# Kernel tuning notes

Hardware: AMD Instinct MI355X
Metric: run time of the kernel (lower is better)

Reference implementation:

```python
import jax, jax.numpy as jnp
import numpy as np
from jax import lax

DIM = 32          # per-head dim of LiteMLA
HEADS = 8         # in_channels // dim = 256 // 32
C = 256           # in_channels = out_channels
EPS = 1e-15       # LiteMLA eps
BN_EPS = 1e-5


def hswish(x):
    return x * jnp.clip(x + 3.0, 0.0, 6.0) / 6.0


def bn(x, g, b, m, v):
    # eval-mode BatchNorm2d folded to per-channel scale/shift
    inv = g / jnp.sqrt(v + BN_EPS)
    return x * inv[None, :, None, None] + (b - m * inv)[None, :, None, None]


def dwconv(x, w):
    # depthwise conv, w: (C,1,k,k), stride 1, SAME padding (= padding k//2)
    return lax.conv_general_dilated(x, w, (1, 1), 'SAME',
                                    dimension_numbers=('NCHW', 'OIHW', 'NCHW'),
                                    feature_group_count=x.shape[1])


def relu_linear_att(qkv):
    # qkv: (B, h*3*DIM, H, W) with h = (1+num_scales)*HEADS
    B, Ctot, H, W = qkv.shape
    N = H * W
    qkv = qkv.reshape(B, -1, 3 * DIM, N)                 # (B,h,3d,N)
    q = jax.nn.relu(qkv[:, :, :DIM])                     # (B,h,d,N)
    k = jax.nn.relu(qkv[:, :, DIM:2 * DIM])
    v = qkv[:, :, 2 * DIM:]
    v = jnp.concatenate([v, jnp.ones_like(v[:, :, :1])], axis=2)  # (B,h,d+1,N)
    kv = jnp.einsum('bhdn,bhen->bhde', v, k)             # (B,h,d+1,d)
    out = jnp.einsum('bhde,bhen->bhdn', kv, q)           # (B,h,d+1,N)
    out = out[:, :, :-1] / (out[:, :, -1:] + EPS)        # normalize by denom row
    return out.reshape(B, -1, H, W)


def lite_mla(x, qkv_w, agg_dw_w, agg_pw_w, proj_w, proj_g, proj_b, proj_m, proj_v):
    qkv = jnp.einsum('bchw,oc->bohw', x, qkv_w)          # 1x1 conv -> (B,3C,H,W)
    d = dwconv(qkv, agg_dw_w)                            # depthwise 5x5
    B, _, H, W = d.shape
    g = 3 * HEADS                                        # 24 groups for grouped 1x1
    dg = d.reshape(B, g, -1, H, W)                       # (B,24,32,H,W)
    pw = jnp.einsum('bgihw,goi->bgohw', dg, agg_pw_w).reshape(B, -1, H, W)
    ms_qkv = jnp.concatenate([qkv, pw], axis=1)          # (B,6C,H,W)
    att = relu_linear_att(ms_qkv)                        # (B,2C,H,W)
    out = jnp.einsum('bchw,oc->bohw', att, proj_w)       # 1x1 proj, no bias
    return bn(out, proj_g, proj_b, proj_m, proj_v)


def mbconv(x, inv_w, inv_b, dwc_w, dwc_b, pw_w, pw_g, pw_b, pw_m, pw_v):
    h = hswish(jnp.einsum('bchw,oc->bohw', x, inv_w) + inv_b[None, :, None, None])
    h = hswish(dwconv(h, dwc_w) + dwc_b[None, :, None, None])
    h = jnp.einsum('bchw,oc->bohw', h, pw_w)
    return bn(h, pw_g, pw_b, pw_m, pw_v)


def setup_inputs() -> dict:
    key = jax.random.key(0)
    ks = jax.random.split(key, 12)
    B, H, W = 16, 32, 32
    mid = 4 * C
    return {
        "x": jax.random.normal(ks[0], (B, C, H, W), jnp.float32),
        "y": jax.random.normal(ks[1], (B, C, H, W), jnp.float32),
        "qkv_w": jax.random.normal(ks[2], (3 * C, C), jnp.float32) * 0.05,
        "agg_dw_w": jax.random.normal(ks[3], (3 * C, 1, 5, 5), jnp.float32) * 0.1,
        "agg_pw_w": jax.random.normal(ks[4], (3 * HEADS, C // HEADS, C // HEADS), jnp.float32) * 0.15,
        "proj_w": jax.random.normal(ks[5], (C, 2 * C), jnp.float32) * 0.04,
        "proj_g": jnp.ones((C,), jnp.float32),
        "proj_b": jnp.zeros((C,), jnp.float32),
        "proj_m": jax.random.normal(ks[6], (C,), jnp.float32) * 0.1,
        "proj_v": jnp.ones((C,), jnp.float32),
        "inv_w": jax.random.normal(ks[7], (mid, C), jnp.float32) * 0.06,
        "inv_b": jnp.zeros((mid,), jnp.float32),
        "dwc_w": jax.random.normal(ks[8], (mid, 1, 3, 3), jnp.float32) * 0.2,
        "dwc_b": jnp.zeros((mid,), jnp.float32),
        "pw_w": jax.random.normal(ks[9], (C, mid), jnp.float32) * 0.03,
        "pw_g": jnp.ones((C,), jnp.float32),
        "pw_b": jnp.zeros((C,), jnp.float32),
        "pw_m": jax.random.normal(ks[10], (C,), jnp.float32) * 0.1,
        "pw_v": jnp.ones((C,), jnp.float32),
    }


def reference(x, y, qkv_w, agg_dw_w, agg_pw_w, proj_w, proj_g, proj_b, proj_m, proj_v,
              inv_w, inv_b, dwc_w, dwc_b, pw_w, pw_g, pw_b, pw_m, pw_v):
    def block(t):
        # context module: residual LiteMLA
        t = t + lite_mla(t, qkv_w, agg_dw_w, agg_pw_w, proj_w, proj_g, proj_b, proj_m, proj_v)
        # local module: residual MBConv
        t = t + mbconv(t, inv_w, inv_b, dwc_w, dwc_b, pw_w, pw_g, pw_b, pw_m, pw_v)
        return t
    return block(x) + block(y)
```

## Files before the change

kernel.cpp:

```cpp
#include <hip/hip_runtime.h>
#include <cstddef>

#define NPIX 1024

static constexpr size_t WQKV_OFF  = 0;
static constexpr size_t WPROJ_OFF = 98304;
static constexpr size_t WINV_OFF  = 163840;
static constexpr size_t WPW_OFF   = 294912;
static constexpr size_t BXT_OFF   = 425984;
static constexpr size_t BQKV_OFF  = 4620288;
static constexpr size_t BDPW_OFF  = 17203200;
static constexpr size_t BATT_OFF  = 29786112;
static constexpr size_t BT1T_OFF  = 425984;
static constexpr size_t BH1T_OFF  = 4620288;
static constexpr size_t BH2T_OFF  = 21397504;
static constexpr size_t BATCH_NEED_F = 38174720;
static constexpr size_t XT_OFF    = 425984;
static constexpr size_t QKV_OFF   = 2523136;
static constexpr size_t DPW_OFF   = 8814592;
static constexpr size_t ATT_OFF   = 15106048;
static constexpr size_t T1_OFF    = 21463040;
static constexpr size_t T1T_OFF   = 25657344;
static constexpr size_t H1T_OFF   = 425984;
static constexpr size_t H2T_OFF   = 25657344;

typedef __attribute__((ext_vector_type(8))) short bf16x8;
typedef __attribute__((ext_vector_type(8))) unsigned short u16x8;
typedef __attribute__((ext_vector_type(4))) unsigned short u16x4;
typedef __attribute__((ext_vector_type(4))) float f32x4;

__device__ inline unsigned short f2bf(float f) {
    union { float f; unsigned int u; } v; v.f = f;
    unsigned int u = v.u;
    u += 0x7FFFu + ((u >> 16) & 1u);
    return (unsigned short)(u >> 16);
}
__device__ inline float bf2f(unsigned short u) {
    union { float f; unsigned int u; } v; v.u = ((unsigned int)u) << 16;
    return v.f;
}
__device__ inline u16x8 zero8() {
    u16x8 z = {0, 0, 0, 0, 0, 0, 0, 0};
    return z;
}

__global__ __launch_bounds__(256)
void wconv_all(const float* __restrict__ w0, const float* __restrict__ w1,
               const float* __restrict__ w2, const float* __restrict__ w3,
               unsigned short* __restrict__ d0, unsigned short* __restrict__ d1,
               unsigned short* __restrict__ d2, unsigned short* __restrict__ d3)
{
    const int bid = blockIdx.x;
    const float* W; unsigned short* WB; int O, K, base;
    if (bid < 96)       { W = w0; WB = d0; O = 768;  K = 256;  base = 0;   }
    else if (bid < 160) { W = w1; WB = d1; O = 256;  K = 512;  base = 96;  }
    else if (bid < 288) { W = w2; WB = d2; O = 1024; K = 256;  base = 160; }
    else                { W = w3; WB = d3; O = 256;  K = 1024; base = 288; }
    const int idx = (bid - base) * 256 + threadIdx.x;
    if (idx >= O * (K >> 3)) return;
    const int o = idx % O;
    const int koct = idx / O;
    u16x8 v;
#pragma unroll
    for (int j = 0; j < 8; j++) v[j] = f2bf(W[(size_t)o * K + koct * 8 + j]);
    *(u16x8*)(WB + ((size_t)koct * O + o) * 8) = v;
}

__global__ __launch_bounds__(256)
void xpose2(const float* __restrict__ X0, const float* __restrict__ X1,
            unsigned short* __restrict__ XT, const int C)
{
    __shared__ float tt[8][260];
    const int t = threadIdx.x;
    const int octs = C >> 3;
    const int strips = octs * 4;
    const int ib = blockIdx.x / strips;
    const int rem = blockIdx.x - ib * strips;
    const int coct = rem >> 2;
    const int n0 = (rem & 3) * 256;
    const float* src = (ib < 16) ? X0 + (size_t)ib * C * NPIX
                                 : X1 + (size_t)(ib - 16) * C * NPIX;
    const int cc = t >> 5;
    const int c8 = (t & 31) * 8;
    const float* xp = src + ((size_t)(coct * 8 + cc)) * NPIX + n0 + c8;
    *(float4*)(&tt[cc][c8])     = *(const float4*)(xp);
    *(float4*)(&tt[cc][c8 + 4]) = *(const float4*)(xp + 4);
    __syncthreads();
    u16x8 v;
#pragma unroll
    for (int j = 0; j < 8; j++) v[j] = f2bf(tt[j][t]);
    *(u16x8*)(XT + (((size_t)ib * octs + coct) * NPIX + n0 + t) * 8) = v;
}

template<int BM, int BN, int EPI, bool ACC, int OMODE>
__global__ __launch_bounds__(256)
void gemm_direct(const unsigned short* __restrict__ X, const unsigned short* __restrict__ X2,
                 const unsigned short* __restrict__ W,
                 float* __restrict__ Y, unsigned short* __restrict__ YB,
                 const int O, const int K,
                 const float* __restrict__ res, const float* __restrict__ res2,
                 const unsigned short* __restrict__ resb,
                 const float* __restrict__ bng, const float* __restrict__ bnb,
                 const float* __restrict__ bnm, const float* __restrict__ bnv,
                 const float* __restrict__ bias)
{
    constexpr int TN = NPIX / BN;
    constexpr int WAVES_N = (BN >= 128) ? 2 : 1;
    constexpr int WM = BM / (4 / WAVES_N);
    constexpr int MI = WM / 16;
    constexpr int NJ = 4;
    constexpr int DEPTH = (MI >= 4) ? 2 : ((EPI == 3 && MI >= 2) ? 2 : 4);

    const int t    = threadIdx.x;
    const int lane = t & 63;
    const int w    = t >> 6;

    const int gx  = gridDim.x;
    const int nwg = gx * gridDim.y;
    int bid = blockIdx.y * gx + blockIdx.x;
    bid = (bid & 7) * (nwg >> 3) + (bid >> 3);
    const int bx = bid % gx;
    const int by = bid / gx;

    const int o0 = bx * BM;
    const int b  = by / TN;
    const int n0 = (by % TN) * BN;

    const int wn = (WAVES_N == 2) ? (w & 1) * 64 : 0;
    const int wo = (WAVES_N == 2) ? (w >> 1) * WM : w * WM;

    const int l16 = lane & 15;
    const int lq  = lane >> 4;

    f32x4 acc[MI][NJ];
    f32x4 acc2[MI][NJ];
#pragma unroll
    for (int i = 0; i < MI; i++)
#pragma unroll
        for (int j = 0; j < NJ; j++) {
            f32x4 z = {0.f, 0.f, 0.f, 0.f};
            acc[i][j] = z;
            acc2[i][j] = z;
        }

    const unsigned short* Ab = W + ((size_t)lq * O + o0 + wo + l16) * 8;
    const size_t strideA = (size_t)O * 8;
    const size_t strideB = (size_t)NPIX * 8;
    const size_t boff = ((size_t)lq * NPIX + n0 + wn + l16) * 8;
    const int octs = K >> 3;

    auto ldA_ = [&](bf16x8* fr, int kb) {
#pragma unroll
        for (int i = 0; i < MI; i++)
            fr[i] = *(const bf16x8*)(Ab + (size_t)kb * strideA + i * 128);
    };
    auto ldB_ = [&](bf16x8* fr, const unsigned short* Bb, int kb) {
#pragma unroll
        for (int j = 0; j < NJ; j++)
            fr[j] = *(const bf16x8*)(Bb + (size_t)kb * strideB + j * 128);
    };
    auto domfma_ = [&](f32x4 (&ac)[MI][NJ], bf16x8* af, bf16x8* bf) {
#pragma unroll
        for (int i = 0; i < MI; i++)
#pragma unroll
            for (int j = 0; j < NJ; j++)
                ac[i][j] = __builtin_amdgcn_mfma_f32_16x16x32_bf16(
                    af[i], bf[j], ac[i][j], 0, 0, 0);
    };

    {
        const unsigned short* B1 = X + (size_t)b * K * NPIX + boff;
        const unsigned short* B2 = (EPI == 3)
            ? X2 + (size_t)b * K * NPIX + boff : nullptr;
        bf16x8 aS[DEPTH][MI], bS[DEPTH][NJ], qS[DEPTH][NJ];
#pragma unroll
        for (int d = 0; d < DEPTH; d++) {
            ldA_(aS[d], d * 4);
            ldB_(bS[d], B1, d * 4);
            if (EPI == 3) ldB_(qS[d], B2, d * 4);
        }
        for (int kb = 0; kb < octs; kb += 4 * DEPTH) {
#pragma unroll
            for (int d = 0; d < DEPTH; d++) {
                domfma_(acc, aS[d], bS[d]);
                if (EPI == 3) domfma_(acc2, aS[d], qS[d]);
                const int nxt = kb + (DEPTH + d) * 4;
                if (nxt < octs) {
                    ldA_(aS[d], nxt);
                    ldB_(bS[d], B1, nxt);
                    if (EPI == 3) ldB_(qS[d], B2, nxt);
                }
            }
        }
    }

    const int r0q = lq * 4;
    float scale[MI][4], shift[MI][4];
    if (EPI == 1 || EPI == 3) {
#pragma unroll
        for (int i = 0; i < MI; i++)
#pragma unroll
            for (int r = 0; r < 4; r++) {
                const int o = o0 + wo + i * 16 + r0q + r;
                const float inv = bng[o] / sqrtf(bnv[o] + 1e-5f);
                scale[i][r] = inv;
                shift[i][r] = bnb[o] - bnm[o] * inv;
            }
    } else if (EPI == 2) {
#pragma unroll
        for (int i = 0; i < MI; i++)
#pragma unroll
            for (int r = 0; r < 4; r++)
                shift[i][r] = bias[o0 + wo + i * 16 + r0q + r];
    }

#pragma unroll
    for (int i = 0; i < MI; i++) {
#pragma unroll
        for (int j = 0; j < NJ; j++) {
            const int nn = n0 + wn + j * 16 + l16;
            const int ob = wo + i * 16 + r0q;
            const size_t base = ((size_t)b * O + o0 + ob) * NPIX + nn;
            u16x4 r1v, r2v;
            if (EPI == 3) {
                const size_t ro = (((size_t)(b * 32 + ((o0 + ob) >> 3)) * NPIX + nn) * 8
                                   + ((o0 + ob) & 7));
                r1v = *(const u16x4*)(resb + ro);
                r2v = *(const u16x4*)(resb + (size_t)16 * 262144 + ro);
            }
            u16x4 p4;
#pragma unroll
            for (int r = 0; r < 4; r++) {
                const size_t off = base + (size_t)r * NPIX;
                float v = acc[i][j][r];
                if (EPI == 1) {
                    const float* rs = (b < 16) ? res : res2;
                    const size_t roff = ((size_t)(b & 15) * O + o0 + ob + r) * NPIX + nn;
                    v = v * scale[i][r] + shift[i][r] + rs[roff];
                } else if (EPI == 2) {
                    v += shift[i][r];
                    v = v * fminf(fmaxf(v + 3.f, 0.f), 6.f) * (1.f / 6.f);
                } else if (EPI == 3) {
                    v = (v + acc2[i][j][r]) * scale[i][r] + 2.f * shift[i][r]
                        + bf2f(r1v[r]) + bf2f(r2v[r]);
                }
                if (OMODE == 0 || OMODE == 3) {
                    if (ACC) v += Y[off];
                    Y[off] = v;
                }
                if (OMODE == 1) {
                    YB[off] = f2bf(v);
                } else if (OMODE >= 2) {
                    p4[r] = f2bf(v);
                }
            }
            if (OMODE >= 2) {
                const int oct = (o0 + ob) >> 3;
                const int sub = (o0 + ob) & 7;
                *(u16x4*)(YB + (((size_t)b * (O >> 3) + oct) * NPIX + nn) * 8 + sub) = p4;
            }
        }
    }
}

__global__ __launch_bounds__(256)
void dwconv5x5_v3(const unsigned short* __restrict__ X, const float* __restrict__ Wd,
                  unsigned short* __restrict__ Y)
{
    __shared__ float tile[2 * 36 * 44];
    __shared__ float wl[64];
    const int t     = threadIdx.x;
    const int cpair = blockIdx.x % 384;
    const int b     = blockIdx.x / 384;
    const int cbase = cpair * 2;
    const unsigned short* xp = X + ((size_t)b * 768 + cbase) * NPIX;

#pragma unroll
    for (int k = 0; k < 4; k++) {
        const int i = t + k * 256;
        if (i < 792) {
            f32x4 z = {0.f, 0.f, 0.f, 0.f};
            *(f32x4*)(&tile[i * 4]) = z;
        }
    }
    if (t < 50) wl[(t / 25) * 32 + (t % 25)] = Wd[cbase * 25 + t];
    __syncthreads();

    const int ch = t >> 7;
    const int tm = t & 127;
    const int r  = tm >> 2;
    const int c8 = (tm & 3) * 8;

    {
        const u16x8 v = *(const u16x8*)(xp + (size_t)ch * NPIX + r * 32 + c8);
        float* wp = &tile[ch * 1584 + (r + 2) * 44 + c8 + 2];
#pragma unroll
        for (int j = 0; j < 8; j += 2) {
            float2 f2v = make_float2(bf2f(v[j]), bf2f(v[j + 1]));
            *(float2*)(wp + j) = f2v;
        }
    }
    float wk[25];
#pragma unroll
    for (int i = 0; i < 25; i++) wk[i] = wl[ch * 32 + i];
    __syncthreads();

    float acc[8];
#pragma unroll
    for (int j = 0; j < 8; j++) acc[j] = 0.f;

#pragma unroll
    for (int ky = 0; ky < 5; ky++) {
        const float* rp = &tile[ch * 1584 + (r + ky) * 44 + c8];
        const f32x4 a = *(const f32x4*)(rp);
        const f32x4 bq = *(const f32x4*)(rp + 4);
        const f32x4 cq = *(const f32x4*)(rp + 8);
        const float in[12] = {a[0], a[1], a[2], a[3], bq[0], bq[1], bq[2], bq[3],
                              cq[0], cq[1], cq[2], cq[3]};
#pragma unroll
        for (int kx = 0; kx < 5; kx++) {
            const float wv = wk[ky * 5 + kx];
#pragma unroll
            for (int j = 0; j < 8; j++)
                acc[j] = fmaf(in[j + kx], wv, acc[j]);
        }
    }

    u16x8 o8;
#pragma unroll
    for (int j = 0; j < 8; j++) o8[j] = f2bf(acc[j]);
    *(u16x8*)(Y + ((size_t)b * 768 + cbase + ch) * NPIX + r * 32 + c8) = o8;
}

__global__ __launch_bounds__(256)
void dwconv3x3_h2(const unsigned short* __restrict__ X, const float* __restrict__ Wd,
                  const float* __restrict__ bias, unsigned short* __restrict__ Y)
{
    __shared__ float wl[72];
    __shared__ float bb[8];
    const int t    = threadIdx.x;
    const int bid  = blockIdx.x;
    const int half = bid & 1;
    const int coct = (bid >> 1) & 127;
    const int b    = bid >> 8;
    const unsigned short* xp = X + ((size_t)(b * 128 + coct)) * NPIX * 8;
    if (t < 72) wl[t] = Wd[coct * 72 + t];
    if (t < 8)  bb[t] = bias[coct * 8 + t];
    __syncthreads();

    const int px0 = half * 512 + t * 2;
    const int hr  = px0 >> 5;
    const int c0  = px0 & 31;

    float acc[8][2];
#pragma unroll
    for (int ch = 0; ch < 8; ch++) {
        acc[ch][0] = bb[ch];
        acc[ch][1] = bb[ch];
    }

#pragma unroll
    for (int ky = 0; ky < 3; ky++) {
        const int rr = hr + ky - 1;
        if (rr >= 0 && rr < 32) {
            u16x8 P[4];
#pragma unroll
            for (int m = 0; m < 4; m++) {
                const int col = c0 - 1 + m;
                const int colc = col < 0 ? 0 : (col > 31 ? 31 : col);
                u16x8 v = *(const u16x8*)(xp + (size_t)(rr * 32 + colc) * 8);
                if (col < 0 || col > 31) v = zero8();
                P[m] = v;
            }
#pragma unroll
            for (int ch = 0; ch < 8; ch++) {
                float g[4];
#pragma unroll
                for (int m = 0; m < 4; m++) g[m] = bf2f(P[m][ch]);
#pragma unroll
                for (int j = 0; j < 2; j++)
#pragma unroll
                    for (int kx = 0; kx < 3; kx++)
                        acc[ch][j] = fmaf(g[j + kx], wl[ch * 9 + ky * 3 + kx], acc[ch][j]);
            }
        }
    }
    unsigned short* yp = Y + ((size_t)(b * 128 + coct)) * NPIX * 8 + (size_t)px0 * 8;
#pragma unroll
    for (int j = 0; j < 2; j++) {
        u16x8 o8;
#pragma unroll
        for (int ch = 0; ch < 8; ch++) {
            float v = acc[ch][j];
            v = v * fminf(fmaxf(v + 3.f, 0.f), 6.f) * (1.f / 6.f);
            o8[ch] = f2bf(v);
        }
        *(u16x8*)(yp + j * 8) = o8;
    }
}

__global__ __launch_bounds__(256)
void grouped_mfma(unsigned short* __restrict__ D, const float* __restrict__ Wg)
{
    const int t    = threadIdx.x;
    const int lane = t & 63;
    const int w    = t >> 6;
    const int bg   = blockIdx.x;
    const int g    = bg % 24;
    const int b    = bg / 24;
    const int l16  = lane & 15;
    const int lq   = lane >> 4;
    const int ko   = lq * 8;
    const int nb   = w * 256;

    unsigned short* dp = D + ((size_t)(b * 768 + g * 32)) * NPIX;

    bf16x8 a0, a1;
#pragma unroll
    for (int j = 0; j < 8; j++) {
        a0[j] = (short)f2bf(Wg[g * 1024 + l16 * 32 + ko + j]);
        a1[j] = (short)f2bf(Wg[g * 1024 + (16 + l16) * 32 + ko + j]);
    }

    bf16x8 bfr[16];
    const unsigned short* ib = dp + (size_t)ko * NPIX + nb + l16;
#pragma unroll
    for (int tl = 0; tl < 16; tl++) {
        bf16x8 bf;
#pragma unroll
        for (int j = 0; j < 8; j++)
            bf[j] = (short)ib[(size_t)j * NPIX + tl * 16];
        bfr[tl] = bf;
    }

    const int ro = lq * 4;
#pragma unroll
    for (int tl = 0; tl < 16; tl++) {
        f32x4 c0 = {0.f, 0.f, 0.f, 0.f};
        f32x4 c1 = {0.f, 0.f, 0.f, 0.f};
        c0 = __builtin_amdgcn_mfma_f32_16x16x32_bf16(a0, bfr[tl], c0, 0, 0, 0);
        c1 = __builtin_amdgcn_mfma_f32_16x16x32_bf16(a1, bfr[tl], c1, 0, 0, 0);
        const int n = nb + tl * 16 + l16;
#pragma unroll
        for (int r = 0; r < 4; r++) {
            dp[(size_t)(ro + r) * NPIX + n]        = f2bf(c0[r]);
            dp[(size_t)(16 + ro + r) * NPIX + n]   = f2bf(c1[r]);
        }
    }
}

__global__ __launch_bounds__(512)
void attn_fused(const unsigned short* __restrict__ qkv,
                const unsigned short* __restrict__ dpw,
                unsigned short* __restrict__ att)
{
    __shared__ float kvred[8][33 * 33];
    __shared__ float kvs[1056];

    const int t    = threadIdx.x;
    const int lane = t & 63;
    const int w    = t >> 6;
    const int bh   = blockIdx.x;
    const int b    = bh >> 4;
    const int h    = bh & 15;

    const unsigned short* base = (h < 8)
        ? qkv + ((size_t)(b * 768 + h * 96)) * NPIX
        : dpw + ((size_t)(b * 768 + (h - 8) * 96)) * NPIX;
    const unsigned short* qp = base;
    const unsigned short* kp = base + 32 * NPIX;
    const unsigned short* vp = base + 64 * NPIX;

    const int l16 = lane & 15;
    const int lq  = lane >> 4;
    const int ko  = lq * 8;
    const int nb  = w * 128;

    {
        f32x4 acc[3][2];
#pragma unroll
        for (int i = 0; i < 3; i++)
#pragma unroll
            for (int j = 0; j < 2; j++) {
                f32x4 z = {0.f, 0.f, 0.f, 0.f};
                acc[i][j] = z;
            }
        bf16x8 ones;
#pragma unroll
        for (int j = 0; j < 8; j++) ones[j] = (l16 == 0) ? (short)0x3F80 : (short)0;

#pragma unroll
        for (int s = 0; s < 4; s++) {
            const int n0 = nb + s * 32 + ko;
            const bf16x8 av0 = *(const bf16x8*)(vp + (size_t)l16 * NPIX + n0);
            const bf16x8 av1 = *(const bf16x8*)(vp + (size_t)(16 + l16) * NPIX + n0);
            const u16x8 k0 = *(const u16x8*)(kp + (size_t)l16 * NPIX + n0);
            const u16x8 k1 = *(const u16x8*)(kp + (size_t)(16 + l16) * NPIX + n0);
            bf16x8 bk0, bk1;
#pragma unroll
            for (int j = 0; j < 8; j++) {
                bk0[j] = (k0[j] & 0x8000u) ? (short)0 : (short)k0[j];
                bk1[j] = (k1[j] & 0x8000u) ? (short)0 : (short)k1[j];
            }
            acc[0][0] = __builtin_amdgcn_mfma_f32_16x16x32_bf16(av0,  bk0, acc[0][0], 0, 0, 0);
            acc[0][1] = __builtin_amdgcn_mfma_f32_16x16x32_bf16(av0,  bk1, acc[0][1], 0, 0, 0);
            acc[1][0] = __builtin_amdgcn_mfma_f32_16x16x32_bf16(av1,  bk0, acc[1][0], 0, 0, 0);
            acc[1][1] = __builtin_amdgcn_mfma_f32_16x16x32_bf16(av1,  bk1, acc[1][1], 0, 0, 0);
            acc[2][0] = __builtin_amdgcn_mfma_f32_16x16x32_bf16(ones, bk0, acc[2][0], 0, 0, 0);
            acc[2][1] = __builtin_amdgcn_mfma_f32_16x16x32_bf16(ones, bk1, acc[2][1], 0, 0, 0);
        }
        const int rbase = lq * 4;
#pragma unroll
        for (int dt = 0; dt < 2; dt++)
#pragma unroll
            for (int et = 0; et < 2; et++)
#pragma unroll
                for (int r = 0; r < 4; r++)
                    kvred[w][(dt * 16 + rbase + r) * 33 + et * 16 + l16] = acc[dt][et][r];
        if (rbase == 0) {
#pragma unroll
            for (int et = 0; et < 2; et++)
                kvred[w][32 * 33 + et * 16 + l16] = acc[2][et][0];
        }
    }
    __syncthreads();
#pragma unroll
    for (int k = 0; k < 3; k++) {
        const int idx = t + k * 512;
        if (idx < 1056) {
            const int a = (idx >> 5) * 33 + (idx & 31);
            float s = 0.f;
#pragma unroll
            for (int ww = 0; ww < 8; ww++) s += kvred[ww][a];
            kvs[idx] = s;
        }
    }
    __syncthreads();

    bf16x8 a0, a1, a2;
#pragma unroll
    for (int j = 0; j < 8; j++) {
        a0[j] = (short)f2bf(kvs[l16 * 32 + ko + j]);
        a1[j] = (short)f2bf(kvs[(16 + l16) * 32 + ko + j]);
        a2[j] = (l16 == 0) ? (short)f2bf(kvs[32 * 32 + ko + j]) : (short)0;
    }
    bf16x8 bfr[8];
    const unsigned short* qb = qp + (size_t)ko * NPIX + nb + l16;
#pragma unroll
    for (int tl = 0; tl < 8; tl++) {
        bf16x8 bf;
#pragma unroll
        for (int j = 0; j < 8; j++) {
            const unsigned short v = qb[(size_t)j * NPIX + tl * 16];
            bf[j] = (v & 0x8000u) ? (short)0 : (short)v;
        }
        bfr[tl] = bf;
    }

    const int db0 = lq >> 1;
    const int sub = (lq & 1) * 4;
    unsigned short* ab0 = att + (((size_t)(b * 64 + h * 4 + db0)) * NPIX) * 8 + sub;
    unsigned short* ab1 = att + (((size_t)(b * 64 + h * 4 + 2 + db0)) * NPIX) * 8 + sub;

#pragma unroll
    for (int tl = 0; tl < 8; tl++) {
        f32x4 z = {0.f, 0.f, 0.f, 0.f};
        z = __builtin_amdgcn_mfma_f32_16x16x32_bf16(a2, bfr[tl], z, 0, 0, 0);
        const float den = __shfl(z[0], l16, 64);
        const float inv = 1.f / (den + 1e-15f);
        f32x4 c0 = {0.f, 0.f, 0.f, 0.f};
        f32x4 c1 = {0.f, 0.f, 0.f, 0.f};
        c0 = __builtin_amdgcn_mfma_f32_16x16x32_bf16(a0, bfr[tl], c0, 0, 0, 0);
        c1 = __builtin_amdgcn_mfma_f32_16x16x32_bf16(a1, bfr[tl], c1, 0, 0, 0);
        u16x4 p0, p1;
#pragma unroll
        for (int r = 0; r < 4; r++) {
            p0[r] = f2bf(c0[r] * inv);
            p1[r] = f2bf(c1[r] * inv);
        }
        const size_t n8 = (size_t)(nb + tl * 16 + l16) * 8;
        *(u16x4*)(ab0 + n8) = p0;
        *(u16x4*)(ab1 + n8) = p1;
    }
}

extern "C" void kernel_launch(void* const* d_in, const int* in_sizes, int n_in,
                              void* d_out, int out_size, void* d_ws, size_t ws_size,
                              hipStream_t stream)
{
    (void)in_sizes; (void)n_in; (void)out_size;

    const float* x      = (const float*)d_in[0];
    const float* y      = (const float*)d_in[1];
    const float* qkv_w  = (const float*)d_in[2];
    const float* dw5_w  = (const float*)d_in[3];
    const float* pwg_w  = (const float*)d_in[4];
    const float* proj_w = (const float*)d_in[5];
    const float* proj_g = (const float*)d_in[6];
    const float* proj_b = (const float*)d_in[7];
    const float* proj_m = (const float*)d_in[8];
    const float* proj_v = (const float*)d_in[9];
    const float* inv_w  = (const float*)d_in[10];
    const float* inv_b  = (const float*)d_in[11];
    const float* dwc_w  = (const float*)d_in[12];
    const float* dwc_b  = (const float*)d_in[13];
    const float* pw_w   = (const float*)d_in[14];
    const float* pw_g   = (const float*)d_in[15];
    const float* pw_b   = (const float*)d_in[16];
    const float* pw_m   = (const float*)d_in[17];
    const float* pw_v   = (const float*)d_in[18];

    float* ws = (float*)d_ws;
    unsigned short* wqkv_b  = (unsigned short*)(ws + WQKV_OFF);
    unsigned short* wproj_b = (unsigned short*)(ws + WPROJ_OFF);
    unsigned short* winv_b  = (unsigned short*)(ws + WINV_OFF);
    unsigned short* wpw_b   = (unsigned short*)(ws + WPW_OFF);
    float* out = (float*)d_out;

    wconv_all<<<dim3(416), 256, 0, stream>>>(qkv_w, proj_w, inv_w, pw_w,
                                             wqkv_b, wproj_b, winv_b, wpw_b);

    if (ws_size >= (size_t)BATCH_NEED_F * 4ull) {
        unsigned short* bxt  = (unsigned short*)(ws + BXT_OFF);
        unsigned short* bqkv = (unsigned short*)(ws + BQKV_OFF);
        unsigned short* bdpw = (unsigned short*)(ws + BDPW_OFF);
        unsigned short* batt = (unsigned short*)(ws + BATT_OFF);
        unsigned short* bt1t = (unsigned short*)(ws + BT1T_OFF);
        unsigned short* bh1t = (unsigned short*)(ws + BH1T_OFF);
        unsigned short* bh2t = (unsigned short*)(ws + BH2T_OFF);

        xpose2<<<dim3(4096), 256, 0, stream>>>(x, y, bxt, 256);
        gemm_direct<128, 128, 0, false, 1><<<dim3(6, 256), 256, 0, stream>>>(
            bxt, nullptr, wqkv_b, nullptr, bqkv, 768, 256,
            nullptr, nullptr, nullptr, nullptr, nullptr, nullptr, nullptr, nullptr);
        dwconv5x5_v3<<<dim3(12288), 256, 0, stream>>>(bqkv, dw5_w, bdpw);
        grouped_mfma<<<dim3(768), 256, 0, stream>>>(bdpw, pwg_w);
        attn_fused<<<dim3(512), 512, 0, stream>>>(bqkv, bdpw, batt);
        gemm_direct<64, 64, 1, false, 2><<<dim3(4, 512), 256, 0, stream>>>(
            batt, nullptr, wproj_b, nullptr, bt1t, 256, 512,
            x, y, nullptr, proj_g, proj_b, proj_m, proj_v, nullptr);
        gemm_direct<128, 128, 2, false, 2><<<dim3(8, 256), 256, 0, stream>>>(
            bt1t, nullptr, winv_b, nullptr, bh1t, 1024, 256,
            nullptr, nullptr, nullptr, nullptr, nullptr, nullptr, nullptr, inv_b);
        dwconv3x3_h2<<<dim3(8192), 256, 0, stream>>>(bh1t, dwc_w, dwc_b, bh2t);
        gemm_direct<64, 128, 3, false, 0><<<dim3(4, 128), 256, 0, stream>>>(
            bh2t, bh2t + (size_t)16 * 1024 * 1024, wpw_b, out, nullptr, 256, 1024,
            nullptr, nullptr, bt1t, pw_g, pw_b, pw_m, pw_v, nullptr);
    } else {
        unsigned short* wxt  = (unsigned short*)(ws + XT_OFF);
        unsigned short* wqkv = (unsigned short*)(ws + QKV_OFF);
        unsigned short* wdpw = (unsigned short*)(ws + DPW_OFF);
        unsigned short* watt = (unsigned short*)(ws + ATT_OFF);
        float*          wt1  = ws + T1_OFF;
        unsigned short* wt1t = (unsigned short*)(ws + T1T_OFF);
        unsigned short* wh1t = (unsigned short*)(ws + H1T_OFF);
        unsigned short* wh2t = (unsigned short*)(ws + H2T_OFF);

        for (int blk = 0; blk < 2; blk++) {
            const float* t = (blk == 0) ? x : y;
            xpose2<<<dim3(2048), 256, 0, stream>>>(t, t, wxt, 256);
            gemm_direct<128, 128, 0, false, 1><<<dim3(6, 128), 256, 0, stream>>>(
                wxt, nullptr, wqkv_b, nullptr, wqkv, 768, 256,
                nullptr, nullptr, nullptr, nullptr, nullptr, nullptr, nullptr, nullptr);
            dwconv5x5_v3<<<dim3(6144), 256, 0, stream>>>(wqkv, dw5_w, wdpw);
            grouped_mfma<<<dim3(384), 256, 0, stream>>>(wdpw, pwg_w);
            attn_fused<<<dim3(256), 512, 0, stream>>>(wqkv, wdpw, watt);
            gemm_direct<64, 64, 1, false, 3><<<dim3(4, 256), 256, 0, stream>>>(
                watt, watt, wproj_b, wt1, wt1t, 256, 512,
                t, t, nullptr, proj_g, proj_b, proj_m, proj_v, nullptr);
            gemm_direct<128, 128, 2, false, 2><<<dim3(8, 128), 256, 0, stream>>>(
                wt1t, nullptr, winv_b, nullptr, wh1t, 1024, 256,
                nullptr, nullptr, nullptr, nullptr, nullptr, nullptr, nullptr, inv_b);
            dwconv3x3_h2<<<dim3(4096), 256, 0, stream>>>(wh1t, dwc_w, dwc_b, wh2t);
            if (blk == 0) {
                gemm_direct<64, 64, 1, false, 0><<<dim3(4, 256), 256, 0, stream>>>(
                    wh2t, nullptr, wpw_b, out, nullptr, 256, 1024,
                    wt1, wt1, nullptr, pw_g, pw_b, pw_m, pw_v, nullptr);
            } else {
                gemm_direct<64, 64, 1, true, 0><<<dim3(4, 256), 256, 0, stream>>>(
                    wh2t, nullptr, wpw_b, out, nullptr, 256, 1024,
                    wt1, wt1, nullptr, pw_g, pw_b, pw_m, pw_v, nullptr);
            }
        }
    }
}
```

Measured before the change: 216.5 us.

## Add LDS-staged double-buffered GEMM using direct global-to-LDS loads for qkv and inverted convs

Introduces a new gemm_lds kernel that stages X and W tiles into shared memory with global_load_lds (direct global-to-LDS DMA), using XOR-swizzled layout and double buffering, replacing gemm_direct for the qkv projection and the inverted-bottleneck 1x1 conv. It also remaps block IDs across groups of eight for cache locality. The aim is to cut redundant global/L2 traffic and hide load latency behind MFMA work, at the cost of 64KB LDS per block, which limits occupancy.

```diff
diff --git a/kernel.cpp b/kernel.cpp
--- a/kernel.cpp
+++ b/kernel.cpp
@@ -43,6 +43,10 @@
     u16x8 z = {0, 0, 0, 0, 0, 0, 0, 0};
     return z;
 }
+
+#define GLOAD_LDS16(gp, lp) __builtin_amdgcn_global_load_lds(                  \
+    (const __attribute__((address_space(1))) unsigned int*)(const void*)(gp), \
+    (__attribute__((address_space(3))) unsigned int*)(void*)(lp), 16, 0, 0)
 
 __global__ __launch_bounds__(256)
 void wconv_all(const float* __restrict__ w0, const float* __restrict__ w1,
@@ -90,6 +94,139 @@
 #pragma unroll
     for (int j = 0; j < 8; j++) v[j] = f2bf(tt[j][t]);
     *(u16x8*)(XT + (((size_t)ib * octs + coct) * NPIX + n0 + t) * 8) = v;
+}
+
+template<int EPI, int OMODE>
+__global__ __launch_bounds__(256)
+void gemm_lds(const unsigned short* __restrict__ X, const unsigned short* __restrict__ W,
+              unsigned short* __restrict__ YB, const int O, const int K,
+              const float* __restrict__ bias)
+{
+    __shared__ unsigned short Asm[2][128][64];
+    __shared__ unsigned short Bsm[2][128][64];
+
+    const int t    = threadIdx.x;
+    const int lane = t & 63;
+    const int w    = t >> 6;
+
+    const int gx  = gridDim.x;
+    const int nwg = gx * gridDim.y;
+    int bid = blockIdx.y * gx + blockIdx.x;
+    bid = (bid & 7) * (nwg >> 3) + (bid >> 3);
+    const int bx = bid % gx;
+    const int by = bid / gx;
+
+    const int o0 = bx * 128;
+    const int b  = by >> 3;
+    const int n0 = (by & 7) * 128;
+
+    const int wo = (w >> 1) * 64;
+    const int wn = (w & 1) * 64;
+
+    f32x4 acc[4][4];
+#pragma unroll
+    for (int i = 0; i < 4; i++)
+#pragma unroll
+        for (int j = 0; j < 4; j++) {
+            f32x4 z = {0.f, 0.f, 0.f, 0.f};
+            acc[i][j] = z;
+        }
+
+    const unsigned short* Xb = X + (size_t)b * K * NPIX;
+    const int lr = lane >> 3;
+    const int sp = lane & 7;
+
+    auto stage = [&](int d, int k0) {
+        const int kb = k0 >> 3;
+#pragma unroll
+        for (int i = 0; i < 4; i++) {
+            const int r0 = w * 32 + i * 8;
+            const int r  = r0 + lr;
+            const int sl = sp ^ (r & 7);
+            GLOAD_LDS16(Xb + (((size_t)(kb + sl)) * NPIX + n0 + r) * 8,
+                        &Bsm[d][r0][0]);
+        }
+#pragma unroll
+        for (int i = 0; i < 4; i++) {
+            const int r0 = w * 32 + i * 8;
+            const int r  = r0 + lr;
+            const int sl = sp ^ (r & 7);
+            GLOAD_LDS16(W + (((size_t)(kb + sl)) * O + o0 + r) * 8,
+                        &Asm[d][r0][0]);
+        }
+    };
+
+    stage(0, 0);
+    __syncthreads();
+
+    const int l16 = lane & 15;
+    const int lq  = lane >> 4;
+
+    int cur = 0;
+    for (int k0 = 0; k0 < K; k0 += 64) {
+        if (k0 + 64 < K) stage(cur ^ 1, k0 + 64);
+#pragma unroll
+        for (int kk = 0; kk < 2; kk++) {
+            bf16x8 afr[4], bfr[4];
+#pragma unroll
+            for (int i = 0; i < 4; i++) {
+                const int r = wo + i * 16 + l16;
+                afr[i] = *(const bf16x8*)&Asm[cur][r][((kk * 4 + lq) ^ (r & 7)) * 8];
+            }
+#pragma unroll
+            for (int j = 0; j < 4; j++) {
+                const int r = wn + j * 16 + l16;
+                bfr[j] = *(const bf16x8*)&Bsm[cur][r][((kk * 4 + lq) ^ (r & 7)) * 8];
+            }
+#pragma unroll
+            for (int i = 0; i < 4; i++)
+#pragma unroll
+                for (int j = 0; j < 4; j++)
+                    acc[i][j] = __builtin_amdgcn_mfma_f32_16x16x32_bf16(
+                        afr[i], bfr[j], acc[i][j], 0, 0, 0);
+        }
+        __syncthreads();
+        cur ^= 1;
+    }
+
+    const int r0q = lq * 4;
+    float shift[4][4];
+    if (EPI == 2) {
+#pragma unroll
+        for (int i = 0; i < 4; i++)
+#pragma unroll
+            for (int r = 0; r < 4; r++)
+                shift[i][r] = bias[o0 + wo + i * 16 + r0q + r];
+    }
+
+#pragma unroll
+    for (int i = 0; i < 4; i++) {
+#pragma unroll
+        for (int j = 0; j < 4; j++) {
+            const int nn = n0 + wn + j * 16 + l16;
+            const int ob = wo + i * 16 + r0q;
+            const size_t base = ((size_t)b * O + o0 + ob) * NPIX + nn;
+            u16x4 p4;
+#pragma unroll
+            for (int r = 0; r < 4; r++) {
+                float v = acc[i][j][r];
+                if (EPI == 2) {
+                    v += shift[i][r];
+                    v = v * fminf(fmaxf(v + 3.f, 0.f), 6.f) * (1.f / 6.f);
+                }
+                if (OMODE == 1) {
+                    YB[base + (size_t)r * NPIX] = f2bf(v);
+                } else {
+                    p4[r] = f2bf(v);
+                }
+            }
+            if (OMODE == 2) {
+                const int oct = (o0 + ob) >> 3;
+                const int sub = (o0 + ob) & 7;
+                *(u16x4*)(YB + (((size_t)b * (O >> 3) + oct) * NPIX + nn) * 8 + sub) = p4;
+            }
+        }
+    }
 }
 
 template<int BM, int BN, int EPI, bool ACC, int OMODE>
@@ -630,18 +767,16 @@
         unsigned short* bh2t = (unsigned short*)(ws + BH2T_OFF);
 
         xpose2<<<dim3(4096), 256, 0, stream>>>(x, y, bxt, 256);
-        gemm_direct<128, 128, 0, false, 1><<<dim3(6, 256), 256, 0, stream>>>(
-            bxt, nullptr, wqkv_b, nullptr, bqkv, 768, 256,
-            nullptr, nullptr, nullptr, nullptr, nullptr, nullptr, nullptr, nullptr);
+        gemm_lds<0, 1><<<dim3(6, 256), 256, 0, stream>>>(
+            bxt, wqkv_b, bqkv, 768, 256, nullptr);
         dwconv5x5_v3<<<dim3(12288), 256, 0, stream>>>(bqkv, dw5_w, bdpw);
         grouped_mfma<<<dim3(768), 256, 0, stream>>>(bdpw, pwg_w);
         attn_fused<<<dim3(512), 512, 0, stream>>>(bqkv, bdpw, batt);
         gemm_direct<64, 64, 1, false, 2><<<dim3(4, 512), 256, 0, stream>>>(
             batt, nullptr, wproj_b, nullptr, bt1t, 256, 512,
             x, y, nullptr, proj_g, proj_b, proj_m, proj_v, nullptr);
-        gemm_direct<128, 128, 2, false, 2><<<dim3(8, 256), 256, 0, stream>>>(
-            bt1t, nullptr, winv_b, nullptr, bh1t, 1024, 256,
-            nullptr, nullptr, nullptr, nullptr, nullptr, nullptr, nullptr, inv_b);
+        gemm_lds<2, 2><<<dim3(8, 256), 256, 0, stream>>>(
+            bt1t, winv_b, bh1t, 1024, 256, inv_b);
         dwconv3x3_h2<<<dim3(8192), 256, 0, stream>>>(bh1t, dwc_w, dwc_b, bh2t);
         gemm_direct<64, 128, 3, false, 0><<<dim3(4, 128), 256, 0, stream>>>(
             bh2t, bh2t + (size_t)16 * 1024 * 1024, wpw_b, out, nullptr, 256, 1024,
@@ -659,18 +794,16 @@
         for (int blk = 0; blk < 2; blk++) {
             const float* t = (blk == 0) ? x : y;
             xpose2<<<dim3(2048), 256, 0, stream>>>(t, t, wxt, 256);
-            gemm_direct<128, 128, 0, false, 1><<<dim3(6, 128), 256, 0, stream>>>(
-                wxt, nullptr, wqkv_b, nullptr, wqkv, 768, 256,
-                nullptr, nullptr, nullptr, nullptr, nullptr, nullptr, nullptr, nullptr);
+            gemm_lds<0, 1><<<dim3(6, 128), 256, 0, stream>>>(
+                wxt, wqkv_b, wqkv, 768, 256, nullptr);
             dwconv5x5_v3<<<dim3(6144), 256, 0, stream>>>(wqkv, dw5_w, wdpw);
             grouped_mfma<<<dim3(384), 256, 0, stream>>>(wdpw, pwg_w);
             attn_fused<<<dim3(256), 512, 0, stream>>>(wqkv, wdpw, watt);
             gemm_direct<64, 64, 1, false, 3><<<dim3(4, 256), 256, 0, stream>>>(
                 watt, watt, wproj_b, wt1, wt1t, 256, 512,
                 t, t, nullptr, proj_g, proj_b, proj_m, proj_v, nullptr);
-            gemm_direct<128, 128, 2, false, 2><<<dim3(8, 128), 256, 0, stream>>>(
-                wt1t, nullptr, winv_b, nullptr, wh1t, 1024, 256,
-                nullptr, nullptr, nullptr, nullptr, nullptr, nullptr, nullptr, inv_b);
+            gemm_lds<2, 2><<<dim3(8, 128), 256, 0, stream>>>(
+                wt1t, winv_b, wh1t, 1024, 256, inv_b);
             dwconv3x3_h2<<<dim3(4096), 256, 0, stream>>>(wh1t, dwc_w, dwc_b, wh2t);
             if (blk == 0) {
                 gemm_direct<64, 64, 1, false, 0><<<dim3(4, 256), 256, 0, stream>>>(
```

After: 240.2 us. +10.9%, slower.

## Fuse input fp32-to-bf16 transpose into QKV GEMM reading fp32 directly

Applied to the files above, without the earlier changes.

Removes the separate xpose2 kernel that converted and transposed the fp32 inputs into a bf16 octet layout, and replaces the QKV GEMM with a dedicated kernel that loads fp32 activations strided by NPIX, converts them to bf16 in registers, and feeds MFMA. This drops one launch and one round trip of the transposed input buffer through global memory. The cost is that B-operand loads become scalar strided fp32 reads with per-element conversion, and the output is written with scalar stores, so global load efficiency may suffer.

```diff
diff --git a/kernel.cpp b/kernel.cpp
--- a/kernel.cpp
+++ b/kernel.cpp
@@ -15,7 +15,6 @@
 static constexpr size_t BH1T_OFF  = 4620288;
 static constexpr size_t BH2T_OFF  = 21397504;
 static constexpr size_t BATCH_NEED_F = 38174720;
-static constexpr size_t XT_OFF    = 425984;
 static constexpr size_t QKV_OFF   = 2523136;
 static constexpr size_t DPW_OFF   = 8814592;
 static constexpr size_t ATT_OFF   = 15106048;
@@ -67,29 +66,102 @@
 }
 
 __global__ __launch_bounds__(256)
-void xpose2(const float* __restrict__ X0, const float* __restrict__ X1,
-            unsigned short* __restrict__ XT, const int C)
+void gemm_qkv_f32(const float* __restrict__ X0, const float* __restrict__ X1,
+                  const unsigned short* __restrict__ W,
+                  unsigned short* __restrict__ YB)
 {
-    __shared__ float tt[8][260];
-    const int t = threadIdx.x;
-    const int octs = C >> 3;
-    const int strips = octs * 4;
-    const int ib = blockIdx.x / strips;
-    const int rem = blockIdx.x - ib * strips;
-    const int coct = rem >> 2;
-    const int n0 = (rem & 3) * 256;
-    const float* src = (ib < 16) ? X0 + (size_t)ib * C * NPIX
-                                 : X1 + (size_t)(ib - 16) * C * NPIX;
-    const int cc = t >> 5;
-    const int c8 = (t & 31) * 8;
-    const float* xp = src + ((size_t)(coct * 8 + cc)) * NPIX + n0 + c8;
-    *(float4*)(&tt[cc][c8])     = *(const float4*)(xp);
-    *(float4*)(&tt[cc][c8 + 4]) = *(const float4*)(xp + 4);
-    __syncthreads();
-    u16x8 v;
-#pragma unroll
-    for (int j = 0; j < 8; j++) v[j] = f2bf(tt[j][t]);
-    *(u16x8*)(XT + (((size_t)ib * octs + coct) * NPIX + n0 + t) * 8) = v;
+    constexpr int O = 768;
+    constexpr int K = 256;
+
+    const int t    = threadIdx.x;
+    const int lane = t & 63;
+    const int w    = t >> 6;
+
+    const int gx  = gridDim.x;
+    const int nwg = gx * gridDim.y;
+    int bid = blockIdx.y * gx + blockIdx.x;
+    bid = (bid & 7) * (nwg >> 3) + (bid >> 3);
+    const int bx = bid % gx;
+    const int by = bid / gx;
+
+    const int o0 = bx * 128;
+    const int b  = by >> 3;
+    const int n0 = (by & 7) * 128;
+
+    const int wn = (w & 1) * 64;
+    const int wo = (w >> 1) * 64;
+
+    const int l16 = lane & 15;
+    const int lq  = lane >> 4;
+
+    f32x4 acc[4][4];
+#pragma unroll
+    for (int i = 0; i < 4; i++)
+#pragma unroll
+        for (int j = 0; j < 4; j++) {
+            f32x4 z = {0.f, 0.f, 0.f, 0.f};
+            acc[i][j] = z;
+        }
+
+    const unsigned short* Ab = W + ((size_t)lq * O + o0 + wo + l16) * 8;
+    const size_t strideA = (size_t)O * 8;
+
+    const float* xb = (b < 16) ? X0 + (size_t)b * K * NPIX
+                               : X1 + (size_t)(b - 16) * K * NPIX;
+    const int nlane = n0 + wn + l16;
+
+    auto ldA_ = [&](bf16x8* fr, int kb) {
+#pragma unroll
+        for (int i = 0; i < 4; i++)
+            fr[i] = *(const bf16x8*)(Ab + (size_t)kb * strideA + i * 128);
+    };
+    auto ldB_ = [&](bf16x8* fr, int kb) {
+        const float* p0 = xb + ((size_t)(kb + lq) * 8) * NPIX + nlane;
+#pragma unroll
+        for (int j = 0; j < 4; j++) {
+            const float* p = p0 + j * 16;
+            bf16x8 f;
+#pragma unroll
+            for (int jj = 0; jj < 8; jj++)
+                f[jj] = (short)f2bf(p[(size_t)jj * NPIX]);
+            fr[j] = f;
+        }
+    };
+    auto domfma_ = [&](bf16x8* af, bf16x8* bf) {
+#pragma unroll
+        for (int i = 0; i < 4; i++)
+#pragma unroll
+            for (int j = 0; j < 4; j++)
+                acc[i][j] = __builtin_amdgcn_mfma_f32_16x16x32_bf16(
+                    af[i], bf[j], acc[i][j], 0, 0, 0);
+    };
+
+    {
+        constexpr int octs = K >> 3;
+        bf16x8 a0[4], a1[4], b0[4], b1[4];
+        ldA_(a0, 0); ldB_(b0, 0);
+        ldA_(a1, 4); ldB_(b1, 4);
+        for (int kb = 0; kb < octs; kb += 8) {
+            domfma_(a0, b0);
+            if (kb + 8 < octs) { ldA_(a0, kb + 8);  ldB_(b0, kb + 8); }
+            domfma_(a1, b1);
+            if (kb + 12 < octs) { ldA_(a1, kb + 12); ldB_(b1, kb + 12); }
+        }
+    }
+
+    const int r0q = lq * 4;
+#pragma unroll
+    for (int i = 0; i < 4; i++) {
+#pragma unroll
+        for (int j = 0; j < 4; j++) {
+            const int nn = n0 + wn + j * 16 + l16;
+            const int ob = wo + i * 16 + r0q;
+            const size_t base = ((size_t)b * O + o0 + ob) * NPIX + nn;
+#pragma unroll
+            for (int r = 0; r < 4; r++)
+                YB[base + (size_t)r * NPIX] = f2bf(acc[i][j][r]);
+        }
+    }
 }
 
 template<int BM, int BN, int EPI, bool ACC, int OMODE>
@@ -621,7 +693,6 @@
                                              wqkv_b, wproj_b, winv_b, wpw_b);
 
     if (ws_size >= (size_t)BATCH_NEED_F * 4ull) {
-        unsigned short* bxt  = (unsigned short*)(ws + BXT_OFF);
         unsigned short* bqkv = (unsigned short*)(ws + BQKV_OFF);
         unsigned short* bdpw = (unsigned short*)(ws + BDPW_OFF);
         unsigned short* batt = (unsigned short*)(ws + BATT_OFF);
@@ -629,10 +700,7 @@
         unsigned short* bh1t = (unsigned short*)(ws + BH1T_OFF);
         unsigned short* bh2t = (unsigned short*)(ws + BH2T_OFF);
 
-        xpose2<<<dim3(4096), 256, 0, stream>>>(x, y, bxt, 256);
-        gemm_direct<128, 128, 0, false, 1><<<dim3(6, 256), 256, 0, stream>>>(
-            bxt, nullptr, wqkv_b, nullptr, bqkv, 768, 256,
-            nullptr, nullptr, nullptr, nullptr, nullptr, nullptr, nullptr, nullptr);
+        gemm_qkv_f32<<<dim3(6, 256), 256, 0, stream>>>(x, y, wqkv_b, bqkv);
         dwconv5x5_v3<<<dim3(12288), 256, 0, stream>>>(bqkv, dw5_w, bdpw);
         grouped_mfma<<<dim3(768), 256, 0, stream>>>(bdpw, pwg_w);
         attn_fused<<<dim3(512), 512, 0, stream>>>(bqkv, bdpw, batt);
@@ -647,7 +715,6 @@
             bh2t, bh2t + (size_t)16 * 1024 * 1024, wpw_b, out, nullptr, 256, 1024,
             nullptr, nullptr, bt1t, pw_g, pw_b, pw_m, pw_v, nullptr);
     } else {
-        unsigned short* wxt  = (unsigned short*)(ws + XT_OFF);
         unsigned short* wqkv = (unsigned short*)(ws + QKV_OFF);
         unsigned short* wdpw = (unsigned short*)(ws + DPW_OFF);
         unsigned short* watt = (unsigned short*)(ws + ATT_OFF);
@@ -658,10 +725,7 @@
 
         for (int blk = 0; blk < 2; blk++) {
             const float* t = (blk == 0) ? x : y;
-            xpose2<<<dim3(2048), 256, 0, stream>>>(t, t, wxt, 256);
-            gemm_direct<128, 128, 0, false, 1><<<dim3(6, 128), 256, 0, stream>>>(
-                wxt, nullptr, wqkv_b, nullptr, wqkv, 768, 256,
-                nullptr, nullptr, nullptr, nullptr, nullptr, nullptr, nullptr, nullptr);
+            gemm_qkv_f32<<<dim3(6, 128), 256, 0, stream>>>(t, t, wqkv_b, wqkv);
             dwconv5x5_v3<<<dim3(6144), 256, 0, stream>>>(wqkv, dw5_w, wdpw);
             grouped_mfma<<<dim3(384), 256, 0, stream>>>(wdpw, pwg_w);
             attn_fused<<<dim3(256), 512, 0, stream>>>(wqkv, wdpw, watt);
```

After: 217.3 us. About the same (+0.3%).
